# Performance work log

Hardware: AMD Instinct MI355X
Metric: run time of the kernel (lower is better)

The kernel has to match this reference:

```python
import jax, jax.numpy as jnp
import numpy as np

N, E, F, H, C, K = 100000, 1600000, 512, 256, 64, 10
EPS = 1e-5  # BatchNorm1d default eps


def setup_inputs() -> dict:
    key = jax.random.key(0)
    ks = jax.random.split(key, 8)
    x = jax.random.normal(ks[0], (N, F), jnp.float32)
    # edge list with no self-loops (gcn_norm adds the self-loops itself)
    src = jax.random.randint(ks[1], (E,), 0, N)
    off = jax.random.randint(ks[2], (E,), 1, N)
    dst = (src + off) % N
    edge_index = jnp.stack([src, dst])
    s = lambda k, sh: jax.random.normal(k, sh, jnp.float32) * 0.02
    W0 = s(ks[3], (F, H)); b0 = jnp.zeros((H,), jnp.float32)
    g0 = jnp.ones((H,), jnp.float32); be0 = jnp.zeros((H,), jnp.float32)
    W1 = s(ks[4], (H, H)); b1 = jnp.zeros((H,), jnp.float32)
    g1 = jnp.ones((H,), jnp.float32); be1 = jnp.zeros((H,), jnp.float32)
    W2 = s(ks[5], (H, C)); b2 = jnp.zeros((C,), jnp.float32)
    proj_w = s(ks[6], (C, 1)); proj_b = jnp.zeros((1,), jnp.float32)
    return dict(x=x, W0=W0, b0=b0, g0=g0, be0=be0, W1=W1, b1=b1, g1=g1,
                be1=be1, W2=W2, b2=b2, proj_w=proj_w, proj_b=proj_b,
                edge_index=edge_index)


def _batchnorm(h, gamma, beta):
    # training-mode BN over the node (batch) axis, biased variance like torch
    mu = h.mean(0)
    var = h.var(0)
    return gamma * (h - mu) * jax.lax.rsqrt(var + EPS) + beta


def _prop(x, edge_index, proj_w, proj_b):
    n, c = x.shape
    loop = jnp.arange(n, dtype=edge_index.dtype)
    row = jnp.concatenate([edge_index[0], loop])  # message sources (x_j)
    col = jnp.concatenate([edge_index[1], loop])  # aggregation targets
    w = jnp.ones(row.shape, x.dtype)
    deg = jax.ops.segment_sum(w, col, num_segments=n)
    dis = jnp.where(deg > 0, jax.lax.rsqrt(jnp.maximum(deg, 1.0)) * (deg > 0), 0.0)
    dis = jnp.where(deg > 0, deg ** -0.5, 0.0)
    norm = dis[row] * dis[col]  # symmetric GCN normalization per edge

    def hop(xk, _):
        msgs = norm[:, None] * xk[row]               # gather + scale  [E+N, C]
        xk = jax.ops.segment_sum(msgs, col, num_segments=n)  # scatter-add
        return xk, xk

    _, hops = jax.lax.scan(hop, x, None, length=K)   # [K, N, C]
    pps = jnp.concatenate([x[None], hops], axis=0).transpose(1, 0, 2)  # [N, K+1, C]
    score = jax.nn.sigmoid(pps @ proj_w + proj_b)[..., 0]  # [N, K+1]
    return jnp.einsum('nk,nkc->nc', score, pps)      # [N, C]


def reference(x, W0, b0, g0, be0, W1, b1, g1, be1, W2, b2, proj_w, proj_b,
              edge_index):
    h = jax.nn.relu(_batchnorm(x @ W0 + b0, g0, be0))   # dropout is identity (eval)
    h = jax.nn.relu(_batchnorm(h @ W1 + b1, g1, be1))
    h = h @ W2 + b2                                     # [N, C] logits
    out = _prop(h, edge_index, proj_w, proj_b)
    return jax.nn.log_softmax(out, axis=1)
```

## Files before the change

kernel.cpp:

```cpp
#include <hip/hip_runtime.h>
#include <hip/hip_bf16.h>
#include <math.h>

#define NN 100000
#define FF 512
#define HH 256
#define CC 64
#define KHOPS 10
#define BN_EPS 1e-5f

typedef __bf16 bf16x8 __attribute__((ext_vector_type(8)));
typedef float f32x4 __attribute__((ext_vector_type(4)));
typedef unsigned short ushort8v __attribute__((ext_vector_type(8)));

__device__ __forceinline__ unsigned short f2bf(float f) {
    __bf16 b = (__bf16)f;
    return __builtin_bit_cast(unsigned short, b);
}
__device__ __forceinline__ float bf2f(unsigned short h) {
    unsigned u = ((unsigned)h) << 16;
    return __builtin_bit_cast(float, u);
}
__device__ __forceinline__ float lo16(unsigned u) { return bf2f((unsigned short)(u & 0xFFFF)); }
__device__ __forceinline__ float hi16(unsigned u) { return bf2f((unsigned short)(u >> 16)); }
__device__ __forceinline__ unsigned pk(float a, float b) {
    return ((unsigned)f2bf(b) << 16) | (unsigned)f2bf(a);
}

typedef __attribute__((address_space(1))) const void g_void;
typedef __attribute__((address_space(3))) void l_void;
__device__ __forceinline__ void gl2lds16(const void* g, void* l) {
    __builtin_amdgcn_global_load_lds((g_void*)g, (l_void*)l, 16, 0, 0);
}

__global__ void k_zero(float* p, int n) {
    int i = blockIdx.x * blockDim.x + threadIdx.x;
    if (i < n) p[i] = 0.f;
}

__global__ void k_deg_init(int* deg, int n) {
    int i = blockIdx.x * blockDim.x + threadIdx.x;
    if (i < n) deg[i] = 1;
}

__global__ void k_deg_count(const int* __restrict__ dst, int e, int* deg) {
    for (int i = blockIdx.x * blockDim.x + threadIdx.x; i < e; i += gridDim.x * blockDim.x)
        atomicAdd(&deg[dst[i]], 1);
}

__global__ void k_dis(const int* __restrict__ deg, float* dis, int n) {
    int i = blockIdx.x * blockDim.x + threadIdx.x;
    if (i < n) dis[i] = rsqrtf((float)deg[i]);
}

#define SCAN_B 1024
#define SCAN_NB ((NN + SCAN_B - 1) / SCAN_B)

__global__ void k_scan1(const int* __restrict__ deg, int* __restrict__ part, int n) {
    __shared__ int ls[SCAN_B];
    int i = blockIdx.x * SCAN_B + threadIdx.x;
    ls[threadIdx.x] = (i < n) ? deg[i] - 1 : 0;
    __syncthreads();
    for (int d = SCAN_B / 2; d > 0; d >>= 1) {
        if (threadIdx.x < d) ls[threadIdx.x] += ls[threadIdx.x + d];
        __syncthreads();
    }
    if (threadIdx.x == 0) part[blockIdx.x] = ls[0];
}

__global__ void k_scan2(int* part, int* offs_last, int nb) {
    if (threadIdx.x == 0) {
        int run = 0;
        for (int b = 0; b < nb; b++) { int v = part[b]; part[b] = run; run += v; }
        offs_last[0] = run;
    }
}

__global__ void k_scan3(const int* __restrict__ deg, const int* __restrict__ part,
                        int* __restrict__ offs, int* __restrict__ cur, int n) {
    __shared__ int ls[SCAN_B];
    int i = blockIdx.x * SCAN_B + threadIdx.x;
    int v = (i < n) ? deg[i] - 1 : 0;
    ls[threadIdx.x] = v;
    __syncthreads();
    for (int d = 1; d < SCAN_B; d <<= 1) {
        int t = (threadIdx.x >= d) ? ls[threadIdx.x - d] : 0;
        __syncthreads();
        ls[threadIdx.x] += t;
        __syncthreads();
    }
    if (i < n) {
        int ex = part[blockIdx.x] + ls[threadIdx.x] - v;
        offs[i] = ex;
        cur[i] = ex;
    }
}

__global__ void k_fill(const int* __restrict__ src, const int* __restrict__ dst, int e,
                       const float* __restrict__ dis, int* cursor,
                       int* __restrict__ csrc, float* __restrict__ cw) {
    for (int i = blockIdx.x * blockDim.x + threadIdx.x; i < e; i += gridDim.x * blockDim.x) {
        int d = dst[i];
        int s = src[i];
        int p = atomicAdd(&cursor[d], 1);
        csrc[p] = s;
        cw[p] = dis[s] * dis[d];
    }
}

__global__ void k_wt(const float* __restrict__ W, unsigned short* __restrict__ Wt,
                     int K, int N) {
    int i = blockIdx.x * blockDim.x + threadIdx.x;
    if (i < K * N) {
        int n = i / K;
        int k = i - n * K;
        Wt[i] = f2bf(W[(size_t)k * N + n]);
    }
}

template <int AF32, int BN_, int STATS, int NW>
__global__ __launch_bounds__(NW * 64) void k_gemm_mfma(
    const void* __restrict__ Av, const unsigned short* __restrict__ Bt,
    const float* __restrict__ bias, unsigned short* __restrict__ Cb,
    float* __restrict__ sum, float* __restrict__ sumsq,
    int M, int K, int Nd) {
    constexpr int NT = NW * 64;
    constexpr int WC = (NW == 8) ? 4 : 2;
    constexpr int PWN = BN_ / WC;
    constexpr int NREP = PWN / 16;
    constexpr int ACH = AF32 ? 8 : 4;
    constexpr int AOPS = 128 * ACH / NT;
    constexpr int BOPS = BN_ * 4 / NT;
    constexpr int ASZ = AF32 ? 16384 : 8192;
    __shared__ __align__(16) unsigned char Asb[ASZ];
    __shared__ __align__(16) unsigned char Bsb[BN_ * 64];
    const int tid = threadIdx.x;
    const int lane = tid & 63;
    const int wid = tid >> 6;
    const int wrow = wid / WC, wcol = wid % WC;
    const int row_base = blockIdx.y * 128;
    const int col_base = blockIdx.x * BN_;
    const unsigned char* Abase = (const unsigned char*)Av;
    const size_t arowb = (size_t)K * (AF32 ? 4 : 2);

    f32x4 acc[4][NREP];
#pragma unroll
    for (int m = 0; m < 4; m++)
#pragma unroll
        for (int n = 0; n < NREP; n++)
#pragma unroll
            for (int j = 0; j < 4; j++) acc[m][n][j] = 0.f;

    for (int kt = 0; kt < K; kt += 32) {
#pragma unroll
        for (int i = 0; i < AOPS; ++i) {
            int e = i * NT + tid;
            int r = e / ACH;
            int c = e % ACH;
            int cs = AF32 ? (c ^ (r & 7)) : (c ^ ((r >> 1) & 3));
            int grow = row_base + r;
            if (grow > M - 1) grow = M - 1;
            const void* g = Abase + (size_t)grow * arowb + (size_t)kt * (AF32 ? 4 : 2) + (cs << 4);
            gl2lds16(g, Asb + e * 16);
        }
#pragma unroll
        for (int i = 0; i < BOPS; ++i) {
            int e = i * NT + tid;
            int r = e >> 2, c = e & 3;
            int cs = c ^ ((r >> 1) & 3);
            const void* g = (const unsigned char*)Bt + (size_t)(col_base + r) * (K * 2) +
                            (size_t)kt * 2 + (cs << 4);
            gl2lds16(g, Bsb + e * 16);
        }
        __syncthreads();

        bf16x8 af[4], bfr[NREP];
#pragma unroll
        for (int m = 0; m < 4; ++m) {
            int r = wrow * 64 + m * 16 + (lane & 15);
            if (AF32) {
                int x7 = r & 7;
                int q2 = (lane >> 4) * 2;
                f32x4 f0 = *(const f32x4*)(Asb + r * 128 + ((q2 ^ x7) << 4));
                f32x4 f1 = *(const f32x4*)(Asb + r * 128 + (((q2 + 1) ^ x7) << 4));
                bf16x8 a;
                a[0] = (__bf16)f0[0]; a[1] = (__bf16)f0[1]; a[2] = (__bf16)f0[2]; a[3] = (__bf16)f0[3];
                a[4] = (__bf16)f1[0]; a[5] = (__bf16)f1[1]; a[6] = (__bf16)f1[2]; a[7] = (__bf16)f1[3];
                af[m] = a;
            } else {
                int cs = (lane >> 4) ^ ((r >> 1) & 3);
                af[m] = *(const bf16x8*)(Asb + r * 64 + (cs << 4));
            }
        }
#pragma unroll
        for (int n = 0; n < NREP; ++n) {
            int r = wcol * PWN + n * 16 + (lane & 15);
            int cs = (lane >> 4) ^ ((r >> 1) & 3);
            bfr[n] = *(const bf16x8*)(Bsb + r * 64 + (cs << 4));
        }
#pragma unroll
        for (int m = 0; m < 4; ++m)
#pragma unroll
            for (int n = 0; n < NREP; ++n)
                acc[m][n] = __builtin_amdgcn_mfma_f32_16x16x32_bf16(af[m], bfr[n], acc[m][n], 0, 0, 0);
        __syncthreads();
    }

    const int lc = lane & 15;
    const int lr = (lane >> 4) * 4;
#pragma unroll
    for (int m = 0; m < 4; ++m) {
        int gr0 = row_base + wrow * 64 + m * 16 + lr;
#pragma unroll
        for (int n = 0; n < NREP; ++n) {
            int gc = col_base + wcol * PWN + n * 16 + lc;
            float bb = bias[gc];
#pragma unroll
            for (int j = 0; j < 4; ++j) {
                int gr = gr0 + j;
                if (gr < M) Cb[(size_t)gr * Nd + gc] = f2bf(acc[m][n][j] + bb);
            }
        }
    }
    if (STATS) {
#pragma unroll
        for (int n = 0; n < NREP; ++n) {
            int gc = col_base + wcol * PWN + n * 16 + lc;
            float bb = bias[gc];
            float s = 0.f, s2 = 0.f;
#pragma unroll
            for (int m = 0; m < 4; ++m) {
                int gr0 = row_base + wrow * 64 + m * 16 + lr;
#pragma unroll
                for (int j = 0; j < 4; ++j) {
                    if (gr0 + j < M) {
                        float v = acc[m][n][j] + bb;
                        s += v;
                        s2 += v * v;
                    }
                }
            }
            s += __shfl_xor(s, 16); s += __shfl_xor(s, 32);
            s2 += __shfl_xor(s2, 16); s2 += __shfl_xor(s2, 32);
            if ((lane >> 4) == 0) {
                atomicAdd(&sum[gc], s);
                atomicAdd(&sumsq[gc], s2);
            }
        }
    }
}

__global__ void k_bnfin(const float* __restrict__ sum, const float* __restrict__ sq,
                        const float* __restrict__ g, const float* __restrict__ be,
                        float* scale, float* shift) {
    int c = threadIdx.x;
    float mu = sum[c] * (1.f / NN);
    float var = sq[c] * (1.f / NN) - mu * mu;
    float sc = g[c] * rsqrtf(var + BN_EPS);
    scale[c] = sc;
    shift[c] = be[c] - mu * sc;
}

__global__ void k_bnapply(unsigned short* __restrict__ h, const float* __restrict__ scale,
                          const float* __restrict__ shift, int n) {
    int total = n * 32;
    for (int idx = blockIdx.x * blockDim.x + threadIdx.x; idx < total;
         idx += gridDim.x * blockDim.x) {
        int c8 = (idx & 31) * 8;
        ushort8v v = *(ushort8v*)(h + (size_t)idx * 8);
        f32x4 s0 = *(const f32x4*)(scale + c8);
        f32x4 s1 = *(const f32x4*)(scale + c8 + 4);
        f32x4 h0 = *(const f32x4*)(shift + c8);
        f32x4 h1 = *(const f32x4*)(shift + c8 + 4);
#pragma unroll
        for (int j = 0; j < 4; j++) {
            v[j] = f2bf(fmaxf(bf2f(v[j]) * s0[j] + h0[j], 0.f));
            v[j + 4] = f2bf(fmaxf(bf2f(v[j + 4]) * s1[j] + h1[j], 0.f));
        }
        *(ushort8v*)(h + (size_t)idx * 8) = v;
    }
}

__global__ void k_hop(const unsigned short* __restrict__ xin,
                      unsigned short* __restrict__ xout,
                      const int* __restrict__ offs, const int* __restrict__ csrc,
                      const float* __restrict__ cw, const float* __restrict__ dis,
                      int n) {
    int wid = (int)((blockIdx.x * (size_t)blockDim.x + threadIdx.x) >> 6);
    if (wid >= n) return;
    int lane = threadIdx.x & 63;
    int g = lane >> 3;
    int j = lane & 7;
    const uint4* x16 = (const uint4*)xin;
    float y0 = 0.f, y1 = 0.f, y2 = 0.f, y3 = 0.f, y4 = 0.f, y5 = 0.f, y6 = 0.f, y7 = 0.f;
    if (g == 0) {
        float dn = dis[wid];
        float w = dn * dn;
        uint4 v = x16[(size_t)wid * 8 + j];
        y0 = w * lo16(v.x); y1 = w * hi16(v.x);
        y2 = w * lo16(v.y); y3 = w * hi16(v.y);
        y4 = w * lo16(v.z); y5 = w * hi16(v.z);
        y6 = w * lo16(v.w); y7 = w * hi16(v.w);
    }
    int p0 = offs[wid], p1 = offs[wid + 1];
    int p = p0 + g;
    for (; p + 8 < p1; p += 16) {
        int sA = csrc[p], sB = csrc[p + 8];
        float wA = cw[p], wB = cw[p + 8];
        uint4 vA = x16[(size_t)sA * 8 + j];
        uint4 vB = x16[(size_t)sB * 8 + j];
        y0 += wA * lo16(vA.x); y1 += wA * hi16(vA.x);
        y2 += wA * lo16(vA.y); y3 += wA * hi16(vA.y);
        y4 += wA * lo16(vA.z); y5 += wA * hi16(vA.z);
        y6 += wA * lo16(vA.w); y7 += wA * hi16(vA.w);
        y0 += wB * lo16(vB.x); y1 += wB * hi16(vB.x);
        y2 += wB * lo16(vB.y); y3 += wB * hi16(vB.y);
        y4 += wB * lo16(vB.z); y5 += wB * hi16(vB.z);
        y6 += wB * lo16(vB.w); y7 += wB * hi16(vB.w);
    }
    for (; p < p1; p += 8) {
        int s = csrc[p];
        float w = cw[p];
        uint4 v = x16[(size_t)s * 8 + j];
        y0 += w * lo16(v.x); y1 += w * hi16(v.x);
        y2 += w * lo16(v.y); y3 += w * hi16(v.y);
        y4 += w * lo16(v.z); y5 += w * hi16(v.z);
        y6 += w * lo16(v.w); y7 += w * hi16(v.w);
    }
#pragma unroll
    for (int m = 8; m <= 32; m <<= 1) {
        y0 += __shfl_xor(y0, m); y1 += __shfl_xor(y1, m);
        y2 += __shfl_xor(y2, m); y3 += __shfl_xor(y3, m);
        y4 += __shfl_xor(y4, m); y5 += __shfl_xor(y5, m);
        y6 += __shfl_xor(y6, m); y7 += __shfl_xor(y7, m);
    }
    if (g == 0) {
        uint4 r;
        r.x = pk(y0, y1); r.y = pk(y2, y3); r.z = pk(y4, y5); r.w = pk(y6, y7);
        ((uint4*)xout)[(size_t)wid * 8 + j] = r;
    }
}

struct XPack { const unsigned short* p[KHOPS + 1]; };

__global__ void k_finprop(XPack xp, const float* __restrict__ pw,
                          const float* __restrict__ pbp, float* __restrict__ out, int n) {
    int gw = (int)((blockIdx.x * (size_t)blockDim.x + threadIdx.x) >> 6);
    int lane = threadIdx.x & 63;
    int hf = lane >> 5;
    int l = lane & 31;
    int node = gw * 2 + hf;
    if (node >= n) return;
    float pw0 = pw[2 * l], pw1 = pw[2 * l + 1];
    float pb0 = pbp[0];
    float o0 = 0.f, o1 = 0.f;
#pragma unroll
    for (int k = 0; k <= KHOPS; k++) {
        unsigned v = ((const unsigned*)xp.p[k])[(size_t)node * 32 + l];
        float v0 = lo16(v);
        float v1 = hi16(v);
        float d = v0 * pw0 + v1 * pw1;
#pragma unroll
        for (int m = 16; m >= 1; m >>= 1) d += __shfl_xor(d, m);
        float s = 1.f / (1.f + expf(-(d + pb0)));
        o0 += s * v0;
        o1 += s * v1;
    }
    float mx = fmaxf(o0, o1);
#pragma unroll
    for (int m = 16; m >= 1; m >>= 1) mx = fmaxf(mx, __shfl_xor(mx, m));
    float e = expf(o0 - mx) + expf(o1 - mx);
#pragma unroll
    for (int m = 16; m >= 1; m >>= 1) e += __shfl_xor(e, m);
    float lg = mx + logf(e);
    float2 r = make_float2(o0 - lg, o1 - lg);
    *(float2*)(out + (size_t)node * 64 + 2 * l) = r;
}

extern "C" void kernel_launch(void* const* d_in, const int* in_sizes, int n_in,
                              void* d_out, int out_size, void* d_ws, size_t ws_size,
                              hipStream_t stream) {
    const float* x  = (const float*)d_in[0];
    const float* W0 = (const float*)d_in[1];
    const float* b0 = (const float*)d_in[2];
    const float* g0 = (const float*)d_in[3];
    const float* be0 = (const float*)d_in[4];
    const float* W1 = (const float*)d_in[5];
    const float* b1 = (const float*)d_in[6];
    const float* g1 = (const float*)d_in[7];
    const float* be1 = (const float*)d_in[8];
    const float* W2 = (const float*)d_in[9];
    const float* b2 = (const float*)d_in[10];
    const float* pw = (const float*)d_in[11];
    const float* pb = (const float*)d_in[12];
    const int* ei = (const int*)d_in[13];
    const int E = in_sizes[13] / 2;
    const int* esrc = ei;
    const int* edst = ei + E;

    char* ws = (char*)d_ws;
    const size_t XKB = (size_t)NN * CC * 2;
    unsigned short* h0b = (unsigned short*)(ws + 0);
    unsigned short* h1b = (unsigned short*)(ws + 51200000);
    unsigned short* xk[KHOPS + 1];
    xk[0] = (unsigned short*)(ws + 0);
    xk[5] = (unsigned short*)(ws + XKB);
    xk[6] = (unsigned short*)(ws + 2 * XKB);
    xk[7] = (unsigned short*)(ws + 3 * XKB);
    xk[1] = (unsigned short*)(ws + 51200000);
    xk[2] = (unsigned short*)(ws + 51200000 + XKB);
    xk[3] = (unsigned short*)(ws + 51200000 + 2 * XKB);
    xk[4] = (unsigned short*)(ws + 51200000 + 3 * XKB);
    xk[8] = (unsigned short*)(ws + 102400000);
    xk[9] = (unsigned short*)(ws + 115200000);
    xk[10] = (unsigned short*)(ws + 128000000);

    int*   deg  = (int*)  (ws + 140800000);
    float* dis  = (float*)(ws + 141200000);
    int*   offs = (int*)  (ws + 141600000);
    int*   cur  = (int*)  (ws + 142000064);
    int*   csrc = (int*)  (ws + 142400064);
    float* cw   = (float*)(ws + 148800064);
    float* stats = (float*)(ws + 155200064);
    int*   part = (int*)  (ws + 155208256);
    unsigned short* W0t = (unsigned short*)(ws + 155209280);
    unsigned short* W1t = (unsigned short*)(ws + 155471424);
    unsigned short* W2t = (unsigned short*)(ws + 155602496);

    float* sum0 = stats,        *sq0 = stats + 256;
    float* sum1 = stats + 512,  *sq1 = stats + 768;
    float* scale0 = stats + 1024, *shift0 = stats + 1280;
    float* scale1 = stats + 1536, *shift1 = stats + 1792;

    float* out = (float*)d_out;

    const int TPB = 256;
    int ngrid = (NN + TPB - 1) / TPB;
    int egrid = (E + TPB - 1) / TPB;
    int wgrid = (NN * 64 + TPB - 1) / TPB;
    int wgrid2 = (((NN + 1) / 2) * 64 + TPB - 1) / TPB;
    int mtiles = (NN + 127) / 128;

    k_zero<<<2, 1024, 0, stream>>>(stats, 2048);
    k_deg_init<<<ngrid, TPB, 0, stream>>>(deg, NN);
    k_deg_count<<<egrid, TPB, 0, stream>>>(edst, E, deg);
    k_dis<<<ngrid, TPB, 0, stream>>>(deg, dis, NN);
    k_scan1<<<SCAN_NB, SCAN_B, 0, stream>>>(deg, part, NN);
    k_scan2<<<1, 64, 0, stream>>>(part, offs + NN, SCAN_NB);
    k_scan3<<<SCAN_NB, SCAN_B, 0, stream>>>(deg, part, offs, cur, NN);
    k_fill<<<egrid, TPB, 0, stream>>>(esrc, edst, E, dis, cur, csrc, cw);

    k_wt<<<(FF * HH + TPB - 1) / TPB, TPB, 0, stream>>>(W0, W0t, FF, HH);
    k_wt<<<(HH * HH + TPB - 1) / TPB, TPB, 0, stream>>>(W1, W1t, HH, HH);
    k_wt<<<(HH * CC + TPB - 1) / TPB, TPB, 0, stream>>>(W2, W2t, HH, CC);

    k_gemm_mfma<1, 256, 1, 8><<<dim3(1, mtiles), 512, 0, stream>>>(
        x, W0t, b0, h0b, sum0, sq0, NN, FF, HH);
    k_bnfin<<<1, 256, 0, stream>>>(sum0, sq0, g0, be0, scale0, shift0);
    k_bnapply<<<2048, TPB, 0, stream>>>(h0b, scale0, shift0, NN);

    k_gemm_mfma<0, 256, 1, 8><<<dim3(1, mtiles), 512, 0, stream>>>(
        h0b, W1t, b1, h1b, sum1, sq1, NN, HH, HH);
    k_bnfin<<<1, 256, 0, stream>>>(sum1, sq1, g1, be1, scale1, shift1);
    k_bnapply<<<2048, TPB, 0, stream>>>(h1b, scale1, shift1, NN);

    k_gemm_mfma<0, 64, 0, 4><<<dim3(1, mtiles), 256, 0, stream>>>(
        h1b, W2t, b2, xk[0], nullptr, nullptr, NN, HH, CC);

    for (int k = 0; k < KHOPS; k++)
        k_hop<<<wgrid, TPB, 0, stream>>>(xk[k], xk[k + 1], offs, csrc, cw, dis, NN);

    XPack xp;
    for (int k = 0; k <= KHOPS; k++) xp.p[k] = xk[k];
    k_finprop<<<wgrid2, TPB, 0, stream>>>(xp, pw, pb, out, NN);
}
```

Baseline: 887.0 us.

## Fuse BN apply into GEMM A-loads, double-buffer GEMM, split hop feature layout

New measurement: 1.266 ms. 42.7% more time.

```diff
diff --git a/kernel.cpp b/kernel.cpp
--- a/kernel.cpp
+++ b/kernel.cpp
@@ -8,6 +8,7 @@
 #define CC 64
 #define KHOPS 10
 #define BN_EPS 1e-5f
+#define SUBX (NN * 16)
 
 typedef __bf16 bf16x8 __attribute__((ext_vector_type(8)));
 typedef float f32x4 __attribute__((ext_vector_type(4)));
@@ -31,6 +32,18 @@
 typedef __attribute__((address_space(3))) void l_void;
 __device__ __forceinline__ void gl2lds16(const void* g, void* l) {
     __builtin_amdgcn_global_load_lds((g_void*)g, (l_void*)l, 16, 0, 0);
+}
+
+template <int N>
+__device__ __forceinline__ void waitcnt_vm() {
+    if constexpr (N == 0) asm volatile("s_waitcnt vmcnt(0)" ::: "memory");
+    else if constexpr (N == 1) asm volatile("s_waitcnt vmcnt(1)" ::: "memory");
+    else if constexpr (N == 2) asm volatile("s_waitcnt vmcnt(2)" ::: "memory");
+    else if constexpr (N == 3) asm volatile("s_waitcnt vmcnt(3)" ::: "memory");
+    else if constexpr (N == 4) asm volatile("s_waitcnt vmcnt(4)" ::: "memory");
+    else if constexpr (N == 5) asm volatile("s_waitcnt vmcnt(5)" ::: "memory");
+    else if constexpr (N == 6) asm volatile("s_waitcnt vmcnt(6)" ::: "memory");
+    else asm volatile("s_waitcnt vmcnt(8)" ::: "memory");
 }
 
 __global__ void k_zero(float* p, int n) {
@@ -118,10 +131,11 @@
     }
 }
 
-template <int AF32, int BN_, int STATS, int NW>
+template <int AF32, int BN_, int STATS, int NW, int FUSEBN, int SPLIT>
 __global__ __launch_bounds__(NW * 64) void k_gemm_mfma(
     const void* __restrict__ Av, const unsigned short* __restrict__ Bt,
     const float* __restrict__ bias, unsigned short* __restrict__ Cb,
+    const float* __restrict__ bnscale, const float* __restrict__ bnshift,
     float* __restrict__ sum, float* __restrict__ sumsq,
     int M, int K, int Nd) {
     constexpr int NT = NW * 64;
@@ -131,9 +145,10 @@
     constexpr int ACH = AF32 ? 8 : 4;
     constexpr int AOPS = 128 * ACH / NT;
     constexpr int BOPS = BN_ * 4 / NT;
-    constexpr int ASZ = AF32 ? 16384 : 8192;
-    __shared__ __align__(16) unsigned char Asb[ASZ];
-    __shared__ __align__(16) unsigned char Bsb[BN_ * 64];
+    constexpr int S = AOPS + BOPS;
+    constexpr int ABUF = AF32 ? 16384 : 8192;
+    __shared__ __align__(16) unsigned char Asb[2][ABUF];
+    __shared__ __align__(16) unsigned char Bsb[2][BN_ * 64];
     const int tid = threadIdx.x;
     const int lane = tid & 63;
     const int wid = tid >> 6;
@@ -151,7 +166,7 @@
 #pragma unroll
             for (int j = 0; j < 4; j++) acc[m][n][j] = 0.f;
 
-    for (int kt = 0; kt < K; kt += 32) {
+    auto stage = [&](int kt, int buf) {
 #pragma unroll
         for (int i = 0; i < AOPS; ++i) {
             int e = i * NT + tid;
@@ -161,7 +176,7 @@
             int grow = row_base + r;
             if (grow > M - 1) grow = M - 1;
             const void* g = Abase + (size_t)grow * arowb + (size_t)kt * (AF32 ? 4 : 2) + (cs << 4);
-            gl2lds16(g, Asb + e * 16);
+            gl2lds16(g, Asb[buf] + e * 16);
         }
 #pragma unroll
         for (int i = 0; i < BOPS; ++i) {
@@ -170,9 +185,28 @@
             int cs = c ^ ((r >> 1) & 3);
             const void* g = (const unsigned char*)Bt + (size_t)(col_base + r) * (K * 2) +
                             (size_t)kt * 2 + (cs << 4);
-            gl2lds16(g, Bsb + e * 16);
-        }
-        __syncthreads();
+            gl2lds16(g, Bsb[buf] + e * 16);
+        }
+    };
+
+    const int nt = K / 32;
+    stage(0, 0);
+    if (nt > 1) stage(32, 1);
+
+    for (int t = 0; t < nt; ++t) {
+        if (t + 1 < nt) waitcnt_vm<S>();
+        else            waitcnt_vm<0>();
+        __builtin_amdgcn_s_barrier();
+        const int cur = t & 1;
+
+        f32x4 sc0{}, sc1{}, sh0{}, sh1{};
+        if (FUSEBN) {
+            int kc = t * 32 + (lane >> 4) * 8;
+            sc0 = *(const f32x4*)(bnscale + kc);
+            sc1 = *(const f32x4*)(bnscale + kc + 4);
+            sh0 = *(const f32x4*)(bnshift + kc);
+            sh1 = *(const f32x4*)(bnshift + kc + 4);
+        }
 
         bf16x8 af[4], bfr[NREP];
 #pragma unroll
@@ -181,29 +215,39 @@
             if (AF32) {
                 int x7 = r & 7;
                 int q2 = (lane >> 4) * 2;
-                f32x4 f0 = *(const f32x4*)(Asb + r * 128 + ((q2 ^ x7) << 4));
-                f32x4 f1 = *(const f32x4*)(Asb + r * 128 + (((q2 + 1) ^ x7) << 4));
+                f32x4 f0 = *(const f32x4*)(Asb[cur] + r * 128 + ((q2 ^ x7) << 4));
+                f32x4 f1 = *(const f32x4*)(Asb[cur] + r * 128 + (((q2 + 1) ^ x7) << 4));
                 bf16x8 a;
                 a[0] = (__bf16)f0[0]; a[1] = (__bf16)f0[1]; a[2] = (__bf16)f0[2]; a[3] = (__bf16)f0[3];
                 a[4] = (__bf16)f1[0]; a[5] = (__bf16)f1[1]; a[6] = (__bf16)f1[2]; a[7] = (__bf16)f1[3];
                 af[m] = a;
             } else {
                 int cs = (lane >> 4) ^ ((r >> 1) & 3);
-                af[m] = *(const bf16x8*)(Asb + r * 64 + (cs << 4));
+                bf16x8 a = *(const bf16x8*)(Asb[cur] + r * 64 + (cs << 4));
+                if (FUSEBN) {
+#pragma unroll
+                    for (int j = 0; j < 4; ++j) {
+                        a[j]     = (__bf16)fmaxf((float)a[j]     * sc0[j] + sh0[j], 0.f);
+                        a[j + 4] = (__bf16)fmaxf((float)a[j + 4] * sc1[j] + sh1[j], 0.f);
+                    }
+                }
+                af[m] = a;
             }
         }
 #pragma unroll
         for (int n = 0; n < NREP; ++n) {
             int r = wcol * PWN + n * 16 + (lane & 15);
             int cs = (lane >> 4) ^ ((r >> 1) & 3);
-            bfr[n] = *(const bf16x8*)(Bsb + r * 64 + (cs << 4));
+            bfr[n] = *(const bf16x8*)(Bsb[cur] + r * 64 + (cs << 4));
         }
 #pragma unroll
         for (int m = 0; m < 4; ++m)
 #pragma unroll
             for (int n = 0; n < NREP; ++n)
                 acc[m][n] = __builtin_amdgcn_mfma_f32_16x16x32_bf16(af[m], bfr[n], acc[m][n], 0, 0, 0);
-        __syncthreads();
+
+        __builtin_amdgcn_s_barrier();
+        if (t + 2 < nt) stage((t + 2) * 32, cur);
     }
 
     const int lc = lane & 15;
@@ -218,7 +262,13 @@
 #pragma unroll
             for (int j = 0; j < 4; ++j) {
                 int gr = gr0 + j;
-                if (gr < M) Cb[(size_t)gr * Nd + gc] = f2bf(acc[m][n][j] + bb);
+                if (gr < M) {
+                    float v = acc[m][n][j] + bb;
+                    if (SPLIT)
+                        Cb[(size_t)(gc >> 4) * SUBX + (size_t)gr * 16 + (gc & 15)] = f2bf(v);
+                    else
+                        Cb[(size_t)gr * Nd + gc] = f2bf(v);
+                }
             }
         }
     }
@@ -261,83 +311,55 @@
     shift[c] = be[c] - mu * sc;
 }
 
-__global__ void k_bnapply(unsigned short* __restrict__ h, const float* __restrict__ scale,
-                          const float* __restrict__ shift, int n) {
-    int total = n * 32;
-    for (int idx = blockIdx.x * blockDim.x + threadIdx.x; idx < total;
-         idx += gridDim.x * blockDim.x) {
-        int c8 = (idx & 31) * 8;
-        ushort8v v = *(ushort8v*)(h + (size_t)idx * 8);
-        f32x4 s0 = *(const f32x4*)(scale + c8);
-        f32x4 s1 = *(const f32x4*)(scale + c8 + 4);
-        f32x4 h0 = *(const f32x4*)(shift + c8);
-        f32x4 h1 = *(const f32x4*)(shift + c8 + 4);
-#pragma unroll
-        for (int j = 0; j < 4; j++) {
-            v[j] = f2bf(fmaxf(bf2f(v[j]) * s0[j] + h0[j], 0.f));
-            v[j + 4] = f2bf(fmaxf(bf2f(v[j + 4]) * s1[j] + h1[j], 0.f));
-        }
-        *(ushort8v*)(h + (size_t)idx * 8) = v;
-    }
-}
-
-__global__ void k_hop(const unsigned short* __restrict__ xin,
-                      unsigned short* __restrict__ xout,
-                      const int* __restrict__ offs, const int* __restrict__ csrc,
-                      const float* __restrict__ cw, const float* __restrict__ dis,
-                      int n) {
-    int wid = (int)((blockIdx.x * (size_t)blockDim.x + threadIdx.x) >> 6);
-    if (wid >= n) return;
+__global__ __launch_bounds__(256) void k_hop4(
+    const unsigned short* __restrict__ xbin, unsigned short* __restrict__ xbout,
+    const int* __restrict__ offs, const int* __restrict__ csrc,
+    const float* __restrict__ cw, const float* __restrict__ dis) {
+    int b = blockIdx.x;
+    int x7 = b & 7;
+    int pass = x7 >> 1;
+    int sub = x7 & 1;
+    int pblk = 2 * (b >> 3) + sub;
+    const uint4* xin = (const uint4*)(xbin + (size_t)pass * SUBX);
+    uint4* xout = (uint4*)(xbout + (size_t)pass * SUBX);
+    int wv = threadIdx.x >> 6;
     int lane = threadIdx.x & 63;
-    int g = lane >> 3;
-    int j = lane & 7;
-    const uint4* x16 = (const uint4*)xin;
+    int q = lane >> 4;
+    int t = lane & 15;
+    int grp = t >> 1, half = t & 1;
+    int node = pblk * 16 + wv * 4 + q;
+
     float y0 = 0.f, y1 = 0.f, y2 = 0.f, y3 = 0.f, y4 = 0.f, y5 = 0.f, y6 = 0.f, y7 = 0.f;
-    if (g == 0) {
-        float dn = dis[wid];
+    if (grp == 0) {
+        float dn = dis[node];
         float w = dn * dn;
-        uint4 v = x16[(size_t)wid * 8 + j];
+        uint4 v = xin[(size_t)node * 2 + half];
         y0 = w * lo16(v.x); y1 = w * hi16(v.x);
         y2 = w * lo16(v.y); y3 = w * hi16(v.y);
         y4 = w * lo16(v.z); y5 = w * hi16(v.z);
         y6 = w * lo16(v.w); y7 = w * hi16(v.w);
     }
-    int p0 = offs[wid], p1 = offs[wid + 1];
-    int p = p0 + g;
-    for (; p + 8 < p1; p += 16) {
-        int sA = csrc[p], sB = csrc[p + 8];
-        float wA = cw[p], wB = cw[p + 8];
-        uint4 vA = x16[(size_t)sA * 8 + j];
-        uint4 vB = x16[(size_t)sB * 8 + j];
-        y0 += wA * lo16(vA.x); y1 += wA * hi16(vA.x);
-        y2 += wA * lo16(vA.y); y3 += wA * hi16(vA.y);
-        y4 += wA * lo16(vA.z); y5 += wA * hi16(vA.z);
-        y6 += wA * lo16(vA.w); y7 += wA * hi16(vA.w);
-        y0 += wB * lo16(vB.x); y1 += wB * hi16(vB.x);
-        y2 += wB * lo16(vB.y); y3 += wB * hi16(vB.y);
-        y4 += wB * lo16(vB.z); y5 += wB * hi16(vB.z);
-        y6 += wB * lo16(vB.w); y7 += wB * hi16(vB.w);
-    }
-    for (; p < p1; p += 8) {
-        int s = csrc[p];
-        float w = cw[p];
-        uint4 v = x16[(size_t)s * 8 + j];
+    int p1 = offs[node + 1];
+    for (int p = offs[node] + grp; p < p1; p += 8) {
+        int s = __builtin_nontemporal_load(&csrc[p]);
+        float w = __builtin_nontemporal_load(&cw[p]);
+        uint4 v = xin[(size_t)s * 2 + half];
         y0 += w * lo16(v.x); y1 += w * hi16(v.x);
         y2 += w * lo16(v.y); y3 += w * hi16(v.y);
         y4 += w * lo16(v.z); y5 += w * hi16(v.z);
         y6 += w * lo16(v.w); y7 += w * hi16(v.w);
     }
 #pragma unroll
-    for (int m = 8; m <= 32; m <<= 1) {
+    for (int m = 2; m <= 8; m <<= 1) {
         y0 += __shfl_xor(y0, m); y1 += __shfl_xor(y1, m);
         y2 += __shfl_xor(y2, m); y3 += __shfl_xor(y3, m);
         y4 += __shfl_xor(y4, m); y5 += __shfl_xor(y5, m);
         y6 += __shfl_xor(y6, m); y7 += __shfl_xor(y7, m);
     }
-    if (g == 0) {
+    if (grp == 0) {
         uint4 r;
         r.x = pk(y0, y1); r.y = pk(y2, y3); r.z = pk(y4, y5); r.w = pk(y6, y7);
-        ((uint4*)xout)[(size_t)wid * 8 + j] = r;
+        xout[(size_t)node * 2 + half] = r;
     }
 }
 
@@ -353,10 +375,11 @@
     if (node >= n) return;
     float pw0 = pw[2 * l], pw1 = pw[2 * l + 1];
     float pb0 = pbp[0];
+    size_t idx = (size_t)(l >> 3) * (SUBX / 2) + (size_t)node * 8 + (l & 7);
     float o0 = 0.f, o1 = 0.f;
 #pragma unroll
     for (int k = 0; k <= KHOPS; k++) {
-        unsigned v = ((const unsigned*)xp.p[k])[(size_t)node * 32 + l];
+        unsigned v = ((const unsigned*)xp.p[k])[idx];
         float v0 = lo16(v);
         float v1 = hi16(v);
         float d = v0 * pw0 + v1 * pw1;
@@ -437,7 +460,6 @@
     const int TPB = 256;
     int ngrid = (NN + TPB - 1) / TPB;
     int egrid = (E + TPB - 1) / TPB;
-    int wgrid = (NN * 64 + TPB - 1) / TPB;
     int wgrid2 = (((NN + 1) / 2) * 64 + TPB - 1) / TPB;
     int mtiles = (NN + 127) / 128;
 
@@ -454,21 +476,19 @@
     k_wt<<<(HH * HH + TPB - 1) / TPB, TPB, 0, stream>>>(W1, W1t, HH, HH);
     k_wt<<<(HH * CC + TPB - 1) / TPB, TPB, 0, stream>>>(W2, W2t, HH, CC);
 
-    k_gemm_mfma<1, 256, 1, 8><<<dim3(1, mtiles), 512, 0, stream>>>(
-        x, W0t, b0, h0b, sum0, sq0, NN, FF, HH);
+    k_gemm_mfma<1, 256, 1, 8, 0, 0><<<dim3(1, mtiles), 512, 0, stream>>>(
+        x, W0t, b0, h0b, nullptr, nullptr, sum0, sq0, NN, FF, HH);
     k_bnfin<<<1, 256, 0, stream>>>(sum0, sq0, g0, be0, scale0, shift0);
-    k_bnapply<<<2048, TPB, 0, stream>>>(h0b, scale0, shift0, NN);
-
-    k_gemm_mfma<0, 256, 1, 8><<<dim3(1, mtiles), 512, 0, stream>>>(
-        h0b, W1t, b1, h1b, sum1, sq1, NN, HH, HH);
+
+    k_gemm_mfma<0, 256, 1, 8, 1, 0><<<dim3(1, mtiles), 512, 0, stream>>>(
+        h0b, W1t, b1, h1b, scale0, shift0, sum1, sq1, NN, HH, HH);
     k_bnfin<<<1, 256, 0, stream>>>(sum1, sq1, g1, be1, scale1, shift1);
-    k_bnapply<<<2048, TPB, 0, stream>>>(h1b, scale1, shift1, NN);
-
-    k_gemm_mfma<0, 64, 0, 4><<<dim3(1, mtiles), 256, 0, stream>>>(
-        h1b, W2t, b2, xk[0], nullptr, nullptr, NN, HH, CC);
+
+    k_gemm_mfma<0, 64, 0, 4, 1, 1><<<dim3(1, mtiles), 256, 0, stream>>>(
+        h1b, W2t, b2, xk[0], scale1, shift1, nullptr, nullptr, NN, HH, CC);
 
     for (int k = 0; k < KHOPS; k++)
-        k_hop<<<wgrid, TPB, 0, stream>>>(xk[k], xk[k + 1], offs, csrc, cw, dis, NN);
+        k_hop4<<<25000, TPB, 0, stream>>>(xk[k], xk[k + 1], offs, csrc, cw, dis);
 
     XPack xp;
     for (int k = 0; k <= KHOPS; k++) xp.p[k] = xk[k];
```
